# Performance work log

Measured on AMD Instinct MI355X. Metric: run time of the kernel, lower is better.

## Reference

```python
import jax, jax.numpy as jnp
import numpy as np

E, D, H = 8, 512, 2048  # num_experts, features, features*mlp_ratio
B, S = 4, 512


def _lecun(key, shape):
    fan_in = shape[-2] if len(shape) >= 2 else shape[0]
    return jax.random.normal(key, shape, dtype=jnp.float32) / jnp.sqrt(jnp.float32(fan_in))


def setup_inputs() -> dict:
    key = jax.random.key(0)
    ks = jax.random.split(key, 8)
    return {
        'x_real': jax.random.normal(ks[0], (B, S, D), dtype=jnp.float32),
        'x_imag': jax.random.normal(ks[1], (B, S, D), dtype=jnp.float32),
        # gating Dense over concat([amp, phase]) -> in_features = 2*D
        'gate_W': _lecun(ks[2], (2 * D, E)),
        'gate_b': jnp.zeros((E,), jnp.float32),
        # per-expert ComplexLinear 1: D -> H
        'W1r': _lecun(ks[3], (E, D, H)),
        'W1i': _lecun(ks[4], (E, D, H)),
        'b1r': jnp.zeros((E, H), jnp.float32),
        'b1i': jnp.zeros((E, H), jnp.float32),
        # per-expert ComplexModReLU bias
        'mod_b': jnp.zeros((E, H), jnp.float32),
        # per-expert ComplexLinear 2: H -> D
        'W2r': _lecun(ks[5], (E, H, D)),
        'W2i': _lecun(ks[6], (E, H, D)),
        'b2r': jnp.zeros((E, D), jnp.float32),
        'b2i': jnp.zeros((E, D), jnp.float32),
    }


def reference(x_real, x_imag, gate_W, gate_b, W1r, W1i, b1r, b1i, mod_b, W2r, W2i, b2r, b2i):
    eps = 1e-10
    # --- gating: scores over [|z|, angle(z)] ---
    amp = jnp.sqrt(x_real ** 2 + x_imag ** 2)            # |z|, [B,S,D]
    phase = jnp.arctan2(x_imag, x_real)                  # angle(z)
    routing_input = jnp.concatenate([amp, phase], axis=-1)  # [B,S,2D]
    scores = routing_input @ gate_W + gate_b             # [B,S,E]
    probs = jax.nn.softmax(scores, axis=-1)
    idx = jnp.argmax(probs, axis=-1)                     # [B,S] top-1 expert

    # --- all experts dense (faithful to reference): complex linear 1 ---
    # (Wr + iWi)(xr + ixi) : hr = xr Wr - xi Wi ; hi = xr Wi + xi Wr
    h_r = (jnp.einsum('bsd,edh->ebsh', x_real, W1r)
           - jnp.einsum('bsd,edh->ebsh', x_imag, W1i)) + b1r[:, None, None, :]
    h_i = (jnp.einsum('bsd,edh->ebsh', x_real, W1i)
           + jnp.einsum('bsd,edh->ebsh', x_imag, W1r)) + b1i[:, None, None, :]

    # --- ComplexModReLU: relu(|z|+b) * z / (|z|+eps), |z| = sqrt(r^2+i^2+eps) ---
    a = jnp.sqrt(h_r ** 2 + h_i ** 2 + eps)              # [E,B,S,H]
    scale = jax.nn.relu(a + mod_b[:, None, None, :]) / (a + eps)
    h_r = h_r * scale
    h_i = h_i * scale

    # --- complex linear 2 ---
    o_r = (jnp.einsum('ebsh,ehd->ebsd', h_r, W2r)
           - jnp.einsum('ebsh,ehd->ebsd', h_i, W2i)) + b2r[:, None, None, :]
    o_i = (jnp.einsum('ebsh,ehd->ebsd', h_r, W2i)
           + jnp.einsum('ebsh,ehd->ebsd', h_i, W2r)) + b2i[:, None, None, :]

    # --- mask + weight (top-1): out = sum_e out_e * probs[...,e] * (argmax==e) ---
    e_ids = jnp.arange(probs.shape[-1])
    w = jnp.transpose(probs, (2, 0, 1)) * (idx[None, :, :] == e_ids[:, None, None])  # [E,B,S]
    out_r = jnp.einsum('ebs,ebsd->bsd', w, o_r)
    out_i = jnp.einsum('ebs,ebsd->bsd', w, o_i)
    return (out_r, out_i)
```

## Files before the change

### kernel.cpp

```cpp
#include <hip/hip_runtime.h>
#include <math.h>

#define NE 8
#define ND 512
#define NH 2048
#define NT 2048

typedef __attribute__((ext_vector_type(8))) short short8;
typedef __attribute__((ext_vector_type(4))) float f32x4;

#define GLL(g, d) __builtin_amdgcn_global_load_lds( \
    (const __attribute__((address_space(1))) void*)(g), \
    (__attribute__((address_space(3))) void*)(d), 16, 0, 0)

__device__ __forceinline__ unsigned short f2bf(float x) {
    unsigned int u = __builtin_bit_cast(unsigned int, x);
    u += 0x7FFFu + ((u >> 16) & 1u);
    return (unsigned short)(u >> 16);
}

__device__ __forceinline__ short8 neg8(short8 v) {
    int4 u = __builtin_bit_cast(int4, v);
    u.x ^= 0x80008000; u.y ^= 0x80008000; u.z ^= 0x80008000; u.w ^= 0x80008000;
    return __builtin_bit_cast(short8, u);
}

__device__ __forceinline__ short8 lds8(const unsigned short* p) {
    return *(const short8*)p;
}

__global__ __launch_bounds__(256) void gate_kernel(
    const float* __restrict__ xr, const float* __restrict__ xi,
    const float* __restrict__ gW, const float* __restrict__ gb,
    float* __restrict__ gate_w,
    int* __restrict__ counts, int* __restrict__ tok_list)
{
    int t = blockIdx.x;
    int tid = threadIdx.x;
    const float* xrt = xr + (size_t)t * ND;
    const float* xit = xi + (size_t)t * ND;

    float acc[NE] = {0,0,0,0,0,0,0,0};
    for (int r = tid; r < 2 * ND; r += 256) {
        int d = r & (ND - 1);
        float a = xrt[d], b = xit[d];
        float v = (r < ND) ? sqrtf(a * a + b * b) : atan2f(b, a);
        const float4* g = (const float4*)(gW + (size_t)r * NE);
        float4 g0 = g[0], g1 = g[1];
        acc[0] += v * g0.x; acc[1] += v * g0.y; acc[2] += v * g0.z; acc[3] += v * g0.w;
        acc[4] += v * g1.x; acc[5] += v * g1.y; acc[6] += v * g1.z; acc[7] += v * g1.w;
    }
    #pragma unroll
    for (int e = 0; e < NE; e++) {
        for (int off = 32; off > 0; off >>= 1)
            acc[e] += __shfl_down(acc[e], off, 64);
    }
    __shared__ float part[4][NE];
    int wave = tid >> 6, lane = tid & 63;
    if (lane == 0) {
        #pragma unroll
        for (int e = 0; e < NE; e++) part[wave][e] = acc[e];
    }
    __syncthreads();
    if (tid == 0) {
        float s[NE];
        #pragma unroll
        for (int e = 0; e < NE; e++)
            s[e] = part[0][e] + part[1][e] + part[2][e] + part[3][e] + gb[e];
        int amax = 0; float m = s[0];
        #pragma unroll
        for (int e = 1; e < NE; e++) if (s[e] > m) { m = s[e]; amax = e; }
        float denom = 0.f;
        #pragma unroll
        for (int e = 0; e < NE; e++) denom += expf(s[e] - m);
        gate_w[t] = 1.0f / denom;
        int pos = atomicAdd(&counts[amax], 1);
        tok_list[amax * NT + pos] = t;
    }
}

__global__ __launch_bounds__(256) void convx_kernel(
    const float* __restrict__ xr, const float* __restrict__ xi,
    unsigned short* __restrict__ obr, unsigned short* __restrict__ obi)
{
    int i = blockIdx.x * 256 + threadIdx.x;
    float4 vr = ((const float4*)xr)[i];
    float4 vi = ((const float4*)xi)[i];
    ((ushort4*)obr)[i] = make_ushort4(f2bf(vr.x), f2bf(vr.y), f2bf(vr.z), f2bf(vr.w));
    ((ushort4*)obi)[i] = make_ushort4(f2bf(vi.x), f2bf(vi.y), f2bf(vi.z), f2bf(vi.w));
}

__global__ __launch_bounds__(256) void transw_kernel(
    const float* __restrict__ s0, unsigned short* __restrict__ d0,
    const float* __restrict__ s1, unsigned short* __restrict__ d1,
    int R, int C)
{
    __shared__ float tile[64][65];
    int e = blockIdx.z;
    int c0 = blockIdx.x * 64, r0 = blockIdx.y * 64;
    size_t off = (size_t)e * R * C;
    int tid = threadIdx.x;
    #pragma unroll
    for (int p = 0; p < 2; ++p) {
        const float* src = (p ? s1 : s0) + off;
        unsigned short* dst = (p ? d1 : d0) + off;
        if (p) __syncthreads();
        for (int i = 0; i < 16; ++i) {
            int idx = tid + i * 256;
            int r = idx >> 6, c = idx & 63;
            tile[r][c] = src[(size_t)(r0 + r) * C + c0 + c];
        }
        __syncthreads();
        for (int i = 0; i < 16; ++i) {
            int idx = tid + i * 256;
            int c = idx >> 6, r = idx & 63;
            dst[(size_t)(c0 + c) * R + r0 + r] = f2bf(tile[r][c]);
        }
    }
}

__global__ __launch_bounds__(256) void moe1_kernel(
    const unsigned short* __restrict__ xbr, const unsigned short* __restrict__ xbi,
    const unsigned short* __restrict__ w1tr, const unsigned short* __restrict__ w1ti,
    const float* __restrict__ b1r, const float* __restrict__ b1i,
    const float* __restrict__ mod_b,
    const int* __restrict__ counts, const int* __restrict__ tok_list,
    unsigned short* __restrict__ hr, unsigned short* __restrict__ hi)
{
    int e = blockIdx.z;
    int n = counts[e];
    int mbase = blockIdx.y * 64;
    if (mbase >= n) return;
    int n0 = blockIdx.x * 128;
    int tid = threadIdx.x;
    int w = tid >> 6, l = tid & 63;
    int l15 = l & 15, quad = l >> 4;

    __shared__ unsigned short sAr[64 * 64];
    __shared__ unsigned short sAi[64 * 64];
    __shared__ unsigned short sBr[128 * 64];
    __shared__ unsigned short sBi[128 * 64];
    __shared__ int toks[64];

    const int* tl = tok_list + e * NT;
    if (tid < 64) {
        int idx = mbase + tid;
        toks[tid] = tl[idx < n ? idx : n - 1];
    }
    __syncthreads();

    int lk = (l & 7) * 8;
    int ra0 = toks[w * 16 + (l >> 3)];
    int ra1 = toks[w * 16 + 8 + (l >> 3)];
    const unsigned short* gAr0 = xbr + (size_t)ra0 * ND + lk;
    const unsigned short* gAi0 = xbi + (size_t)ra0 * ND + lk;
    const unsigned short* gAr1 = xbr + (size_t)ra1 * ND + lk;
    const unsigned short* gAi1 = xbi + (size_t)ra1 * ND + lk;
    size_t brow = (size_t)e * NH + n0 + w * 32 + (l >> 3);
    const unsigned short* gBr0 = w1tr + (brow +  0) * ND + lk;
    const unsigned short* gBr1 = w1tr + (brow +  8) * ND + lk;
    const unsigned short* gBr2 = w1tr + (brow + 16) * ND + lk;
    const unsigned short* gBr3 = w1tr + (brow + 24) * ND + lk;
    const unsigned short* gBi0 = w1ti + (brow +  0) * ND + lk;
    const unsigned short* gBi1 = w1ti + (brow +  8) * ND + lk;
    const unsigned short* gBi2 = w1ti + (brow + 16) * ND + lk;
    const unsigned short* gBi3 = w1ti + (brow + 24) * ND + lk;

    unsigned short* dAr0 = sAr + (w * 16) * 64;
    unsigned short* dAr1 = sAr + (w * 16 + 8) * 64;
    unsigned short* dAi0 = sAi + (w * 16) * 64;
    unsigned short* dAi1 = sAi + (w * 16 + 8) * 64;
    unsigned short* dBr0 = sBr + (w * 32) * 64;
    unsigned short* dBr1 = sBr + (w * 32 + 8) * 64;
    unsigned short* dBr2 = sBr + (w * 32 + 16) * 64;
    unsigned short* dBr3 = sBr + (w * 32 + 24) * 64;
    unsigned short* dBi0 = sBi + (w * 32) * 64;
    unsigned short* dBi1 = sBi + (w * 32 + 8) * 64;
    unsigned short* dBi2 = sBi + (w * 32 + 16) * 64;
    unsigned short* dBi3 = sBi + (w * 32 + 24) * 64;

    f32x4 accr[4][2] = {}, acci[4][2] = {};

    for (int kt = 0; kt < ND / 64; ++kt) {
        __syncthreads();
        int ko = kt * 64;
        GLL(gAr0 + ko, dAr0); GLL(gAi0 + ko, dAi0);
        GLL(gAr1 + ko, dAr1); GLL(gAi1 + ko, dAi1);
        GLL(gBr0 + ko, dBr0); GLL(gBr1 + ko, dBr1);
        GLL(gBr2 + ko, dBr2); GLL(gBr3 + ko, dBr3);
        GLL(gBi0 + ko, dBi0); GLL(gBi1 + ko, dBi1);
        GLL(gBi2 + ko, dBi2); GLL(gBi3 + ko, dBi3);
        __syncthreads();
        #pragma unroll
        for (int ks = 0; ks < 2; ++ks) {
            int kb = ks * 32 + quad * 8;
            short8 ar[4], ai2[4], an[4];
            #pragma unroll
            for (int m = 0; m < 4; ++m) {
                ar[m]  = lds8(sAr + (m * 16 + l15) * 64 + kb);
                ai2[m] = lds8(sAi + (m * 16 + l15) * 64 + kb);
                an[m]  = neg8(ai2[m]);
            }
            short8 br[2], bi2[2];
            #pragma unroll
            for (int t = 0; t < 2; ++t) {
                br[t]  = lds8(sBr + (w * 32 + t * 16 + l15) * 64 + kb);
                bi2[t] = lds8(sBi + (w * 32 + t * 16 + l15) * 64 + kb);
            }
            #pragma unroll
            for (int m = 0; m < 4; ++m)
                #pragma unroll
                for (int t = 0; t < 2; ++t) {
                    accr[m][t] = __builtin_amdgcn_mfma_f32_16x16x32_bf16(ar[m],  br[t],  accr[m][t], 0, 0, 0);
                    accr[m][t] = __builtin_amdgcn_mfma_f32_16x16x32_bf16(an[m],  bi2[t], accr[m][t], 0, 0, 0);
                    acci[m][t] = __builtin_amdgcn_mfma_f32_16x16x32_bf16(ar[m],  bi2[t], acci[m][t], 0, 0, 0);
                    acci[m][t] = __builtin_amdgcn_mfma_f32_16x16x32_bf16(ai2[m], br[t],  acci[m][t], 0, 0, 0);
                }
        }
    }

    #pragma unroll
    for (int t = 0; t < 2; ++t) {
        int col = n0 + w * 32 + t * 16 + l15;
        float bre = b1r[(size_t)e * NH + col];
        float bie = b1i[(size_t)e * NH + col];
        float mbv = mod_b[(size_t)e * NH + col];
        #pragma unroll
        for (int m = 0; m < 4; ++m) {
            #pragma unroll
            for (int r = 0; r < 4; ++r) {
                int tix = m * 16 + quad * 4 + r;
                if (mbase + tix >= n) continue;
                int tok = toks[tix];
                float vr = accr[m][t][r] + bre;
                float vi = acci[m][t][r] + bie;
                float a = sqrtf(vr * vr + vi * vi + 1e-10f);
                float sc = fmaxf(a + mbv, 0.0f) / (a + 1e-10f);
                hr[(size_t)tok * NH + col] = f2bf(vr * sc);
                hi[(size_t)tok * NH + col] = f2bf(vi * sc);
            }
        }
    }
}

__global__ __launch_bounds__(256) void moe2_kernel(
    const unsigned short* __restrict__ hr, const unsigned short* __restrict__ hi,
    const unsigned short* __restrict__ w2tr, const unsigned short* __restrict__ w2ti,
    const float* __restrict__ b2r, const float* __restrict__ b2i,
    const int* __restrict__ counts, const int* __restrict__ tok_list,
    const float* __restrict__ gate_w,
    float* __restrict__ out)
{
    int e = blockIdx.z;
    int n = counts[e];
    int mbase = blockIdx.y * 64;
    if (mbase >= n) return;
    int n0 = blockIdx.x * 64;
    int tid = threadIdx.x;
    int w = tid >> 6, l = tid & 63;
    int l15 = l & 15, quad = l >> 4;

    __shared__ unsigned short sAr[64 * 64];
    __shared__ unsigned short sAi[64 * 64];
    __shared__ unsigned short sBr[64 * 64];
    __shared__ unsigned short sBi[64 * 64];
    __shared__ int toks[64];

    const int* tl = tok_list + e * NT;
    if (tid < 64) {
        int idx = mbase + tid;
        toks[tid] = tl[idx < n ? idx : n - 1];
    }
    __syncthreads();

    int lk = (l & 7) * 8;
    int ra0 = toks[w * 16 + (l >> 3)];
    int ra1 = toks[w * 16 + 8 + (l >> 3)];
    const unsigned short* gAr0 = hr + (size_t)ra0 * NH + lk;
    const unsigned short* gAi0 = hi + (size_t)ra0 * NH + lk;
    const unsigned short* gAr1 = hr + (size_t)ra1 * NH + lk;
    const unsigned short* gAi1 = hi + (size_t)ra1 * NH + lk;
    size_t brow = (size_t)e * ND + n0 + w * 16 + (l >> 3);
    const unsigned short* gBr0 = w2tr + (brow + 0) * NH + lk;
    const unsigned short* gBr1 = w2tr + (brow + 8) * NH + lk;
    const unsigned short* gBi0 = w2ti + (brow + 0) * NH + lk;
    const unsigned short* gBi1 = w2ti + (brow + 8) * NH + lk;

    unsigned short* dAr0 = sAr + (w * 16) * 64;
    unsigned short* dAr1 = sAr + (w * 16 + 8) * 64;
    unsigned short* dAi0 = sAi + (w * 16) * 64;
    unsigned short* dAi1 = sAi + (w * 16 + 8) * 64;
    unsigned short* dBr0 = sBr + (w * 16) * 64;
    unsigned short* dBr1 = sBr + (w * 16 + 8) * 64;
    unsigned short* dBi0 = sBi + (w * 16) * 64;
    unsigned short* dBi1 = sBi + (w * 16 + 8) * 64;

    f32x4 accr[4] = {}, acci[4] = {};

    for (int kt = 0; kt < NH / 64; ++kt) {
        __syncthreads();
        int ko = kt * 64;
        GLL(gAr0 + ko, dAr0); GLL(gAi0 + ko, dAi0);
        GLL(gAr1 + ko, dAr1); GLL(gAi1 + ko, dAi1);
        GLL(gBr0 + ko, dBr0); GLL(gBr1 + ko, dBr1);
        GLL(gBi0 + ko, dBi0); GLL(gBi1 + ko, dBi1);
        __syncthreads();
        #pragma unroll
        for (int ks = 0; ks < 2; ++ks) {
            int kb = ks * 32 + quad * 8;
            short8 br = lds8(sBr + (w * 16 + l15) * 64 + kb);
            short8 bi2 = lds8(sBi + (w * 16 + l15) * 64 + kb);
            #pragma unroll
            for (int m = 0; m < 4; ++m) {
                short8 ar  = lds8(sAr + (m * 16 + l15) * 64 + kb);
                short8 ai2 = lds8(sAi + (m * 16 + l15) * 64 + kb);
                short8 an  = neg8(ai2);
                accr[m] = __builtin_amdgcn_mfma_f32_16x16x32_bf16(ar,  br,  accr[m], 0, 0, 0);
                accr[m] = __builtin_amdgcn_mfma_f32_16x16x32_bf16(an,  bi2, accr[m], 0, 0, 0);
                acci[m] = __builtin_amdgcn_mfma_f32_16x16x32_bf16(ar,  bi2, acci[m], 0, 0, 0);
                acci[m] = __builtin_amdgcn_mfma_f32_16x16x32_bf16(ai2, br,  acci[m], 0, 0, 0);
            }
        }
    }

    int col = n0 + w * 16 + l15;
    float bre = b2r[(size_t)e * ND + col];
    float bie = b2i[(size_t)e * ND + col];
    #pragma unroll
    for (int m = 0; m < 4; ++m) {
        #pragma unroll
        for (int r = 0; r < 4; ++r) {
            int tix = m * 16 + quad * 4 + r;
            if (mbase + tix >= n) continue;
            int tok = toks[tix];
            float gw = gate_w[tok];
            out[(size_t)tok * ND + col] = (accr[m][r] + bre) * gw;
            out[(size_t)NT * ND + (size_t)tok * ND + col] = (acci[m][r] + bie) * gw;
        }
    }
}

extern "C" void kernel_launch(void* const* d_in, const int* in_sizes, int n_in,
                              void* d_out, int out_size, void* d_ws, size_t ws_size,
                              hipStream_t stream) {
    const float* xr   = (const float*)d_in[0];
    const float* xi   = (const float*)d_in[1];
    const float* gW   = (const float*)d_in[2];
    const float* gb   = (const float*)d_in[3];
    const float* W1r  = (const float*)d_in[4];
    const float* W1i  = (const float*)d_in[5];
    const float* b1r  = (const float*)d_in[6];
    const float* b1i  = (const float*)d_in[7];
    const float* modb = (const float*)d_in[8];
    const float* W2r  = (const float*)d_in[9];
    const float* W2i  = (const float*)d_in[10];
    const float* b2r  = (const float*)d_in[11];
    const float* b2i  = (const float*)d_in[12];
    float* out = (float*)d_out;

    char* ws = (char*)d_ws;
    int*   counts   = (int*)ws;
    float* gate_w   = (float*)(ws + 256);
    int*   tok_list = (int*)(ws + 256 + 8192);
    size_t off = 256 + 8192 + (size_t)NE * NT * 4;
    unsigned short* xbr  = (unsigned short*)(ws + off); off += (size_t)NT * ND * 2;
    unsigned short* xbi  = (unsigned short*)(ws + off); off += (size_t)NT * ND * 2;
    unsigned short* w1tr = (unsigned short*)(ws + off); off += (size_t)NE * ND * NH * 2;
    unsigned short* w1ti = (unsigned short*)(ws + off); off += (size_t)NE * ND * NH * 2;
    unsigned short* w2tr = (unsigned short*)(ws + off); off += (size_t)NE * ND * NH * 2;
    unsigned short* w2ti = (unsigned short*)(ws + off); off += (size_t)NE * ND * NH * 2;
    unsigned short* h_r  = (unsigned short*)(ws + off); off += (size_t)NT * NH * 2;
    unsigned short* h_i  = (unsigned short*)(ws + off); off += (size_t)NT * NH * 2;

    hipMemsetAsync(counts, 0, 64 * sizeof(int), stream);
    gate_kernel<<<NT, 256, 0, stream>>>(xr, xi, gW, gb, gate_w, counts, tok_list);
    convx_kernel<<<(NT * ND / 4) / 256, 256, 0, stream>>>(xr, xi, xbr, xbi);
    transw_kernel<<<dim3(NH / 64, ND / 64, NE), 256, 0, stream>>>(W1r, w1tr, W1i, w1ti, ND, NH);
    transw_kernel<<<dim3(ND / 64, NH / 64, NE), 256, 0, stream>>>(W2r, w2tr, W2i, w2ti, NH, ND);
    moe1_kernel<<<dim3(NH / 128, NT / 64, NE), 256, 0, stream>>>(
        xbr, xbi, w1tr, w1ti, b1r, b1i, modb, counts, tok_list, h_r, h_i);
    moe2_kernel<<<dim3(ND / 64, NT / 64, NE), 256, 0, stream>>>(
        h_r, h_i, w2tr, w2ti, b2r, b2i, counts, tok_list, gate_w, out);
}
```

Before: 350.4 us.

## Split-K second expert GEMM with atomics, shrink first GEMM tile, swizzle LDS

The second expert GEMM is split four ways along the hidden dimension, and the partial results are accumulated into a zeroed output with atomicAdd. This raises block count, which matters because most token tiles are empty under top-1 routing. The first GEMM uses a smaller 64-wide N tile, which doubles its grid and halves per-block registers. Both kernels get an XOR swizzle on the LDS column layout to cut bank conflicts, plus occupancy hints in launch_bounds. The costs are an extra output memset, atomic traffic, and nondeterministic summation order.

Result: faster. 314.1 us (-10.3%).

```diff
diff --git a/kernel.cpp b/kernel.cpp
--- a/kernel.cpp
+++ b/kernel.cpp
@@ -119,137 +119,13 @@
     }
 }
 
-__global__ __launch_bounds__(256) void moe1_kernel(
+__global__ __launch_bounds__(256, 4) void moe1_kernel(
     const unsigned short* __restrict__ xbr, const unsigned short* __restrict__ xbi,
     const unsigned short* __restrict__ w1tr, const unsigned short* __restrict__ w1ti,
     const float* __restrict__ b1r, const float* __restrict__ b1i,
     const float* __restrict__ mod_b,
     const int* __restrict__ counts, const int* __restrict__ tok_list,
     unsigned short* __restrict__ hr, unsigned short* __restrict__ hi)
-{
-    int e = blockIdx.z;
-    int n = counts[e];
-    int mbase = blockIdx.y * 64;
-    if (mbase >= n) return;
-    int n0 = blockIdx.x * 128;
-    int tid = threadIdx.x;
-    int w = tid >> 6, l = tid & 63;
-    int l15 = l & 15, quad = l >> 4;
-
-    __shared__ unsigned short sAr[64 * 64];
-    __shared__ unsigned short sAi[64 * 64];
-    __shared__ unsigned short sBr[128 * 64];
-    __shared__ unsigned short sBi[128 * 64];
-    __shared__ int toks[64];
-
-    const int* tl = tok_list + e * NT;
-    if (tid < 64) {
-        int idx = mbase + tid;
-        toks[tid] = tl[idx < n ? idx : n - 1];
-    }
-    __syncthreads();
-
-    int lk = (l & 7) * 8;
-    int ra0 = toks[w * 16 + (l >> 3)];
-    int ra1 = toks[w * 16 + 8 + (l >> 3)];
-    const unsigned short* gAr0 = xbr + (size_t)ra0 * ND + lk;
-    const unsigned short* gAi0 = xbi + (size_t)ra0 * ND + lk;
-    const unsigned short* gAr1 = xbr + (size_t)ra1 * ND + lk;
-    const unsigned short* gAi1 = xbi + (size_t)ra1 * ND + lk;
-    size_t brow = (size_t)e * NH + n0 + w * 32 + (l >> 3);
-    const unsigned short* gBr0 = w1tr + (brow +  0) * ND + lk;
-    const unsigned short* gBr1 = w1tr + (brow +  8) * ND + lk;
-    const unsigned short* gBr2 = w1tr + (brow + 16) * ND + lk;
-    const unsigned short* gBr3 = w1tr + (brow + 24) * ND + lk;
-    const unsigned short* gBi0 = w1ti + (brow +  0) * ND + lk;
-    const unsigned short* gBi1 = w1ti + (brow +  8) * ND + lk;
-    const unsigned short* gBi2 = w1ti + (brow + 16) * ND + lk;
-    const unsigned short* gBi3 = w1ti + (brow + 24) * ND + lk;
-
-    unsigned short* dAr0 = sAr + (w * 16) * 64;
-    unsigned short* dAr1 = sAr + (w * 16 + 8) * 64;
-    unsigned short* dAi0 = sAi + (w * 16) * 64;
-    unsigned short* dAi1 = sAi + (w * 16 + 8) * 64;
-    unsigned short* dBr0 = sBr + (w * 32) * 64;
-    unsigned short* dBr1 = sBr + (w * 32 + 8) * 64;
-    unsigned short* dBr2 = sBr + (w * 32 + 16) * 64;
-    unsigned short* dBr3 = sBr + (w * 32 + 24) * 64;
-    unsigned short* dBi0 = sBi + (w * 32) * 64;
-    unsigned short* dBi1 = sBi + (w * 32 + 8) * 64;
-    unsigned short* dBi2 = sBi + (w * 32 + 16) * 64;
-    unsigned short* dBi3 = sBi + (w * 32 + 24) * 64;
-
-    f32x4 accr[4][2] = {}, acci[4][2] = {};
-
-    for (int kt = 0; kt < ND / 64; ++kt) {
-        __syncthreads();
-        int ko = kt * 64;
-        GLL(gAr0 + ko, dAr0); GLL(gAi0 + ko, dAi0);
-        GLL(gAr1 + ko, dAr1); GLL(gAi1 + ko, dAi1);
-        GLL(gBr0 + ko, dBr0); GLL(gBr1 + ko, dBr1);
-        GLL(gBr2 + ko, dBr2); GLL(gBr3 + ko, dBr3);
-        GLL(gBi0 + ko, dBi0); GLL(gBi1 + ko, dBi1);
-        GLL(gBi2 + ko, dBi2); GLL(gBi3 + ko, dBi3);
-        __syncthreads();
-        #pragma unroll
-        for (int ks = 0; ks < 2; ++ks) {
-            int kb = ks * 32 + quad * 8;
-            short8 ar[4], ai2[4], an[4];
-            #pragma unroll
-            for (int m = 0; m < 4; ++m) {
-                ar[m]  = lds8(sAr + (m * 16 + l15) * 64 + kb);
-                ai2[m] = lds8(sAi + (m * 16 + l15) * 64 + kb);
-                an[m]  = neg8(ai2[m]);
-            }
-            short8 br[2], bi2[2];
-            #pragma unroll
-            for (int t = 0; t < 2; ++t) {
-                br[t]  = lds8(sBr + (w * 32 + t * 16 + l15) * 64 + kb);
-                bi2[t] = lds8(sBi + (w * 32 + t * 16 + l15) * 64 + kb);
-            }
-            #pragma unroll
-            for (int m = 0; m < 4; ++m)
-                #pragma unroll
-                for (int t = 0; t < 2; ++t) {
-                    accr[m][t] = __builtin_amdgcn_mfma_f32_16x16x32_bf16(ar[m],  br[t],  accr[m][t], 0, 0, 0);
-                    accr[m][t] = __builtin_amdgcn_mfma_f32_16x16x32_bf16(an[m],  bi2[t], accr[m][t], 0, 0, 0);
-                    acci[m][t] = __builtin_amdgcn_mfma_f32_16x16x32_bf16(ar[m],  bi2[t], acci[m][t], 0, 0, 0);
-                    acci[m][t] = __builtin_amdgcn_mfma_f32_16x16x32_bf16(ai2[m], br[t],  acci[m][t], 0, 0, 0);
-                }
-        }
-    }
-
-    #pragma unroll
-    for (int t = 0; t < 2; ++t) {
-        int col = n0 + w * 32 + t * 16 + l15;
-        float bre = b1r[(size_t)e * NH + col];
-        float bie = b1i[(size_t)e * NH + col];
-        float mbv = mod_b[(size_t)e * NH + col];
-        #pragma unroll
-        for (int m = 0; m < 4; ++m) {
-            #pragma unroll
-            for (int r = 0; r < 4; ++r) {
-                int tix = m * 16 + quad * 4 + r;
-                if (mbase + tix >= n) continue;
-                int tok = toks[tix];
-                float vr = accr[m][t][r] + bre;
-                float vi = acci[m][t][r] + bie;
-                float a = sqrtf(vr * vr + vi * vi + 1e-10f);
-                float sc = fmaxf(a + mbv, 0.0f) / (a + 1e-10f);
-                hr[(size_t)tok * NH + col] = f2bf(vr * sc);
-                hi[(size_t)tok * NH + col] = f2bf(vi * sc);
-            }
-        }
-    }
-}
-
-__global__ __launch_bounds__(256) void moe2_kernel(
-    const unsigned short* __restrict__ hr, const unsigned short* __restrict__ hi,
-    const unsigned short* __restrict__ w2tr, const unsigned short* __restrict__ w2ti,
-    const float* __restrict__ b2r, const float* __restrict__ b2i,
-    const int* __restrict__ counts, const int* __restrict__ tok_list,
-    const float* __restrict__ gate_w,
-    float* __restrict__ out)
 {
     int e = blockIdx.z;
     int n = counts[e];
@@ -273,18 +149,18 @@
     }
     __syncthreads();
 
-    int lk = (l & 7) * 8;
+    int swz = (((l & 7) ^ ((l >> 3) & 7)) * 8);
     int ra0 = toks[w * 16 + (l >> 3)];
     int ra1 = toks[w * 16 + 8 + (l >> 3)];
-    const unsigned short* gAr0 = hr + (size_t)ra0 * NH + lk;
-    const unsigned short* gAi0 = hi + (size_t)ra0 * NH + lk;
-    const unsigned short* gAr1 = hr + (size_t)ra1 * NH + lk;
-    const unsigned short* gAi1 = hi + (size_t)ra1 * NH + lk;
-    size_t brow = (size_t)e * ND + n0 + w * 16 + (l >> 3);
-    const unsigned short* gBr0 = w2tr + (brow + 0) * NH + lk;
-    const unsigned short* gBr1 = w2tr + (brow + 8) * NH + lk;
-    const unsigned short* gBi0 = w2ti + (brow + 0) * NH + lk;
-    const unsigned short* gBi1 = w2ti + (brow + 8) * NH + lk;
+    const unsigned short* gAr0 = xbr + (size_t)ra0 * ND + swz;
+    const unsigned short* gAi0 = xbi + (size_t)ra0 * ND + swz;
+    const unsigned short* gAr1 = xbr + (size_t)ra1 * ND + swz;
+    const unsigned short* gAi1 = xbi + (size_t)ra1 * ND + swz;
+    size_t brow = (size_t)e * NH + n0 + w * 16 + (l >> 3);
+    const unsigned short* gBr0 = w1tr + brow * ND + swz;
+    const unsigned short* gBr1 = w1tr + (brow + 8) * ND + swz;
+    const unsigned short* gBi0 = w1ti + brow * ND + swz;
+    const unsigned short* gBi1 = w1ti + (brow + 8) * ND + swz;
 
     unsigned short* dAr0 = sAr + (w * 16) * 64;
     unsigned short* dAr1 = sAr + (w * 16 + 8) * 64;
@@ -297,7 +173,7 @@
 
     f32x4 accr[4] = {}, acci[4] = {};
 
-    for (int kt = 0; kt < NH / 64; ++kt) {
+    for (int kt = 0; kt < ND / 64; ++kt) {
         __syncthreads();
         int ko = kt * 64;
         GLL(gAr0 + ko, dAr0); GLL(gAi0 + ko, dAi0);
@@ -307,13 +183,13 @@
         __syncthreads();
         #pragma unroll
         for (int ks = 0; ks < 2; ++ks) {
-            int kb = ks * 32 + quad * 8;
-            short8 br = lds8(sBr + (w * 16 + l15) * 64 + kb);
-            short8 bi2 = lds8(sBi + (w * 16 + l15) * 64 + kb);
+            int pa = ((ks * 4 + quad) ^ (l15 & 7)) * 8;
+            short8 br  = lds8(sBr + (w * 16 + l15) * 64 + pa);
+            short8 bi2 = lds8(sBi + (w * 16 + l15) * 64 + pa);
             #pragma unroll
             for (int m = 0; m < 4; ++m) {
-                short8 ar  = lds8(sAr + (m * 16 + l15) * 64 + kb);
-                short8 ai2 = lds8(sAi + (m * 16 + l15) * 64 + kb);
+                short8 ar  = lds8(sAr + (m * 16 + l15) * 64 + pa);
+                short8 ai2 = lds8(sAi + (m * 16 + l15) * 64 + pa);
                 short8 an  = neg8(ai2);
                 accr[m] = __builtin_amdgcn_mfma_f32_16x16x32_bf16(ar,  br,  accr[m], 0, 0, 0);
                 accr[m] = __builtin_amdgcn_mfma_f32_16x16x32_bf16(an,  bi2, accr[m], 0, 0, 0);
@@ -324,8 +200,111 @@
     }
 
     int col = n0 + w * 16 + l15;
-    float bre = b2r[(size_t)e * ND + col];
-    float bie = b2i[(size_t)e * ND + col];
+    float bre = b1r[(size_t)e * NH + col];
+    float bie = b1i[(size_t)e * NH + col];
+    float mbv = mod_b[(size_t)e * NH + col];
+    #pragma unroll
+    for (int m = 0; m < 4; ++m) {
+        #pragma unroll
+        for (int r = 0; r < 4; ++r) {
+            int tix = m * 16 + quad * 4 + r;
+            if (mbase + tix >= n) continue;
+            int tok = toks[tix];
+            float vr = accr[m][r] + bre;
+            float vi = acci[m][r] + bie;
+            float a = sqrtf(vr * vr + vi * vi + 1e-10f);
+            float sc = fmaxf(a + mbv, 0.0f) / (a + 1e-10f);
+            hr[(size_t)tok * NH + col] = f2bf(vr * sc);
+            hi[(size_t)tok * NH + col] = f2bf(vi * sc);
+        }
+    }
+}
+
+__global__ __launch_bounds__(256, 4) void moe2_kernel(
+    const unsigned short* __restrict__ hr, const unsigned short* __restrict__ hi,
+    const unsigned short* __restrict__ w2tr, const unsigned short* __restrict__ w2ti,
+    const float* __restrict__ b2r, const float* __restrict__ b2i,
+    const int* __restrict__ counts, const int* __restrict__ tok_list,
+    const float* __restrict__ gate_w,
+    float* __restrict__ out)
+{
+    int e = blockIdx.z >> 2;
+    int ksl = blockIdx.z & 3;
+    int n = counts[e];
+    int mbase = blockIdx.y * 64;
+    if (mbase >= n) return;
+    int n0 = blockIdx.x * 64;
+    int kbase = ksl * (NH / 4);
+    int tid = threadIdx.x;
+    int w = tid >> 6, l = tid & 63;
+    int l15 = l & 15, quad = l >> 4;
+
+    __shared__ unsigned short sAr[64 * 64];
+    __shared__ unsigned short sAi[64 * 64];
+    __shared__ unsigned short sBr[64 * 64];
+    __shared__ unsigned short sBi[64 * 64];
+    __shared__ int toks[64];
+
+    const int* tl = tok_list + e * NT;
+    if (tid < 64) {
+        int idx = mbase + tid;
+        toks[tid] = tl[idx < n ? idx : n - 1];
+    }
+    __syncthreads();
+
+    int swz = (((l & 7) ^ ((l >> 3) & 7)) * 8);
+    int ra0 = toks[w * 16 + (l >> 3)];
+    int ra1 = toks[w * 16 + 8 + (l >> 3)];
+    const unsigned short* gAr0 = hr + (size_t)ra0 * NH + kbase + swz;
+    const unsigned short* gAi0 = hi + (size_t)ra0 * NH + kbase + swz;
+    const unsigned short* gAr1 = hr + (size_t)ra1 * NH + kbase + swz;
+    const unsigned short* gAi1 = hi + (size_t)ra1 * NH + kbase + swz;
+    size_t brow = (size_t)e * ND + n0 + w * 16 + (l >> 3);
+    const unsigned short* gBr0 = w2tr + brow * NH + kbase + swz;
+    const unsigned short* gBr1 = w2tr + (brow + 8) * NH + kbase + swz;
+    const unsigned short* gBi0 = w2ti + brow * NH + kbase + swz;
+    const unsigned short* gBi1 = w2ti + (brow + 8) * NH + kbase + swz;
+
+    unsigned short* dAr0 = sAr + (w * 16) * 64;
+    unsigned short* dAr1 = sAr + (w * 16 + 8) * 64;
+    unsigned short* dAi0 = sAi + (w * 16) * 64;
+    unsigned short* dAi1 = sAi + (w * 16 + 8) * 64;
+    unsigned short* dBr0 = sBr + (w * 16) * 64;
+    unsigned short* dBr1 = sBr + (w * 16 + 8) * 64;
+    unsigned short* dBi0 = sBi + (w * 16) * 64;
+    unsigned short* dBi1 = sBi + (w * 16 + 8) * 64;
+
+    f32x4 accr[4] = {}, acci[4] = {};
+
+    for (int kt = 0; kt < (NH / 4) / 64; ++kt) {
+        __syncthreads();
+        int ko = kt * 64;
+        GLL(gAr0 + ko, dAr0); GLL(gAi0 + ko, dAi0);
+        GLL(gAr1 + ko, dAr1); GLL(gAi1 + ko, dAi1);
+        GLL(gBr0 + ko, dBr0); GLL(gBr1 + ko, dBr1);
+        GLL(gBi0 + ko, dBi0); GLL(gBi1 + ko, dBi1);
+        __syncthreads();
+        #pragma unroll
+        for (int ks = 0; ks < 2; ++ks) {
+            int pa = ((ks * 4 + quad) ^ (l15 & 7)) * 8;
+            short8 br  = lds8(sBr + (w * 16 + l15) * 64 + pa);
+            short8 bi2 = lds8(sBi + (w * 16 + l15) * 64 + pa);
+            #pragma unroll
+            for (int m = 0; m < 4; ++m) {
+                short8 ar  = lds8(sAr + (m * 16 + l15) * 64 + pa);
+                short8 ai2 = lds8(sAi + (m * 16 + l15) * 64 + pa);
+                short8 an  = neg8(ai2);
+                accr[m] = __builtin_amdgcn_mfma_f32_16x16x32_bf16(ar,  br,  accr[m], 0, 0, 0);
+                accr[m] = __builtin_amdgcn_mfma_f32_16x16x32_bf16(an,  bi2, accr[m], 0, 0, 0);
+                acci[m] = __builtin_amdgcn_mfma_f32_16x16x32_bf16(ar,  bi2, acci[m], 0, 0, 0);
+                acci[m] = __builtin_amdgcn_mfma_f32_16x16x32_bf16(ai2, br,  acci[m], 0, 0, 0);
+            }
+        }
+    }
+
+    int col = n0 + w * 16 + l15;
+    float bre = (ksl == 0) ? b2r[(size_t)e * ND + col] : 0.0f;
+    float bie = (ksl == 0) ? b2i[(size_t)e * ND + col] : 0.0f;
     #pragma unroll
     for (int m = 0; m < 4; ++m) {
         #pragma unroll
@@ -334,8 +313,8 @@
             if (mbase + tix >= n) continue;
             int tok = toks[tix];
             float gw = gate_w[tok];
-            out[(size_t)tok * ND + col] = (accr[m][r] + bre) * gw;
-            out[(size_t)NT * ND + (size_t)tok * ND + col] = (acci[m][r] + bie) * gw;
+            atomicAdd(&out[(size_t)tok * ND + col], (accr[m][r] + bre) * gw);
+            atomicAdd(&out[(size_t)NT * ND + (size_t)tok * ND + col], (acci[m][r] + bie) * gw);
         }
     }
 }
@@ -373,12 +352,13 @@
     unsigned short* h_i  = (unsigned short*)(ws + off); off += (size_t)NT * NH * 2;
 
     hipMemsetAsync(counts, 0, 64 * sizeof(int), stream);
+    hipMemsetAsync(out, 0, (size_t)out_size * sizeof(float), stream);
     gate_kernel<<<NT, 256, 0, stream>>>(xr, xi, gW, gb, gate_w, counts, tok_list);
     convx_kernel<<<(NT * ND / 4) / 256, 256, 0, stream>>>(xr, xi, xbr, xbi);
     transw_kernel<<<dim3(NH / 64, ND / 64, NE), 256, 0, stream>>>(W1r, w1tr, W1i, w1ti, ND, NH);
     transw_kernel<<<dim3(ND / 64, NH / 64, NE), 256, 0, stream>>>(W2r, w2tr, W2i, w2ti, NH, ND);
-    moe1_kernel<<<dim3(NH / 128, NT / 64, NE), 256, 0, stream>>>(
+    moe1_kernel<<<dim3(NH / 64, NT / 64, NE), 256, 0, stream>>>(
         xbr, xbi, w1tr, w1ti, b1r, b1i, modb, counts, tok_list, h_r, h_i);
-    moe2_kernel<<<dim3(ND / 64, NT / 64, NE), 256, 0, stream>>>(
+    moe2_kernel<<<dim3(ND / 64, NT / 64, NE * 4), 256, 0, stream>>>(
         h_r, h_i, w2tr, w2ti, b2r, b2i, counts, tok_list, gate_w, out);
 }
```
